# Kernel tuning notes

Measured on AMD Instinct MI355X. Metric: run time of the kernel, lower is better.

Reference implementation:

```python
import jax, jax.numpy as jnp
import numpy as np

B, N, E, D, H, C, FF, NQ, NCLS = 4, 1024, 512, 256, 2, 128, 1024, 4, 24
K_LOCAL, K_GLOBAL = 8, 7


def _ln(x, g, b, eps=1e-5):
    m = jnp.mean(x, -1, keepdims=True)
    v = jnp.mean((x - m) ** 2, -1, keepdims=True)
    return (x - m) * jax.lax.rsqrt(v + eps) * g + b


def _knn_mask(dist, k, exclude_self):
    # dist: [n, n]; returns bool mask[target, source] of k nearest sources per target
    n = dist.shape[-1]
    d = jnp.where(jnp.eye(n, dtype=bool), 1e9, dist) if exclude_self else dist
    idx = jax.lax.top_k(-d, k)[1]  # [n, k]
    rows = jnp.arange(n)[:, None]
    return jnp.zeros((n, n), dtype=bool).at[rows, idx].set(True)


def _mha(q, k, v, scale, extra_mask=None):
    # q: [B,Lq,H,C]  k,v: [B,Lk,H,C]
    logits = jnp.einsum('bqhc,bkhc->bhqk', q, k) * scale
    if extra_mask is not None:
        logits = logits + extra_mask
    a = jax.nn.softmax(logits, axis=-1)
    return jnp.einsum('bhqk,bkhc->bqhc', a, v)


def _forward(inputs, cellposes, sparse_rand, emb_W, emb_b, pe_tab, pe_W1, pe_b1, pe_W2, pe_b2,
             gat_W, gat_att_src, gat_att_dst, gat_b, ln_g, ln_b,
             tf_qkv_W, tf_qkv_b, tf_out_W, tf_out_b, tf_ff1_W, tf_ff1_b, tf_ff2_W, tf_ff2_b,
             tf_ln1_g, tf_ln1_b, tf_ln2_g, tf_ln2_b,
             query_embed, pool_in_W, pool_in_b, pool_out_W, pool_out_b,
             m1_W, m1_b, m_ln1_g, m_ln1_b, m2_W, m2_b, m_ln2_g, m_ln2_b, m3_W, m3_b,
             c1_W, c1_b, c2_W, c2_b, c3_W, c3_b, c4_W, c4_b, masks):
    # masks are all ones (full bags) -> key_padding_mask is all-False, no padding effect
    x = inputs @ emb_W.T + emb_b                                  # [B,N,D]
    # 2D position embedding: per-coordinate Embedding -> Linear -> ReLU -> Linear
    pos_idx = jnp.clip(cellposes, 0, 1000).astype(jnp.int32)      # [B,N,2]
    pes = []
    for c in range(2):
        e = pe_tab[c][pos_idx[..., c]]                            # [B,N,D//2]
        e = jax.nn.relu(e @ pe_W1[c].T + pe_b1[c]) @ pe_W2[c].T + pe_b2[c]
        pes.append(e)
    x = x + jnp.concatenate(pes, axis=-1)
    # kNN graph: local k=8 with self-loops + global k=7 without; coalesce('max') => edge-set union
    pm = cellposes.mean(axis=1, keepdims=True)
    ps = cellposes.std(axis=1, keepdims=True) + 1e-8
    pn = (cellposes - pm) / ps
    sq = jnp.sum((pn[:, :, None, :] - pn[:, None, :, :]) ** 2, axis=-1)
    dist = jax.lax.stop_gradient(jnp.sqrt(sq + 1e-12))            # [B,N,N]
    local = jax.vmap(lambda d: _knn_mask(d, K_LOCAL, False))(dist)
    glob = jax.vmap(lambda d: _knn_mask(d, K_GLOBAL, True))(dist)
    adj = local | glob                                            # [B, target, source]
    # GAT layers (PyG GATConv; edge weights are ignored since edge_dim=None)
    for l in range(gat_W.shape[0]):
        res = x
        h = (x @ gat_W[l].T).reshape(B, N, H, C)
        a_src = jnp.einsum('bnhc,hc->bnh', h, gat_att_src[l])
        a_dst = jnp.einsum('bnhc,hc->bnh', h, gat_att_dst[l])
        e = jax.nn.leaky_relu(a_dst[:, :, None, :] + a_src[:, None, :, :], 0.2)  # [B,t,s,H]
        e = jnp.where(adj[..., None], e, -1e9)
        a = jax.nn.softmax(e, axis=2)
        out = jnp.einsum('btsh,bshc->bthc', a, h).reshape(B, N, D) + gat_b[l]
        x = _ln(out + res, ln_g, ln_b)
    # TransformerEncoder: post-norm, ReLU FFN, batch_first, eval (no dropout)
    scale = 1.0 / jnp.sqrt(jnp.float32(C))
    for l in range(tf_qkv_W.shape[0]):
        qkv = x @ tf_qkv_W[l].T + tf_qkv_b[l]
        q, k, v = [t.reshape(B, N, H, C) for t in jnp.split(qkv, 3, axis=-1)]
        o = _mha(q, k, v, scale).reshape(B, N, D) @ tf_out_W[l].T + tf_out_b[l]
        x = _ln(x + o, tf_ln1_g[l], tf_ln1_b[l])
        ff = jax.nn.relu(x @ tf_ff1_W[l].T + tf_ff1_b[l]) @ tf_ff2_W[l].T + tf_ff2_b[l]
        x = _ln(x + ff, tf_ln2_g[l], tf_ln2_b[l])
    x = _ln(x, ln_g, ln_b)
    pooled_avg = x.mean(axis=1)                                   # AdaptiveAvgPool1d(1) == mean over seq
    # Sparse multihead attention pooling with learned queries
    queries = jnp.broadcast_to(query_embed[None], (B, NQ, D))
    attn_mask = jnp.where(sparse_rand < 0.3, 0.0, -1e9)           # [NQ, N]
    Wq, Wk, Wv = jnp.split(pool_in_W, 3, axis=0)
    bq, bk, bv = jnp.split(pool_in_b, 3, axis=0)
    q = (queries @ Wq.T + bq).reshape(B, NQ, H, C)
    k = (x @ Wk.T + bk).reshape(B, N, H, C)
    v = (x @ Wv.T + bv).reshape(B, N, H, C)
    pooled_att = _mha(q, k, v, scale, attn_mask[None, None]).reshape(B, NQ, D) @ pool_out_W.T + pool_out_b
    combined = jnp.concatenate([pooled_avg, pooled_att.reshape(B, NQ * D)], axis=-1)  # [B,(1+NQ)*D]
    h = jax.nn.relu(combined @ m1_W.T + m1_b)
    h = _ln(h, m_ln1_g, m_ln1_b)
    h = jax.nn.relu(h @ m2_W.T + m2_b)
    h = _ln(h, m_ln2_g, m_ln2_b)
    h = h @ m3_W.T + m3_b
    h = jax.nn.relu(h @ c1_W.T + c1_b)
    h = jax.nn.relu(h @ c2_W.T + c2_b)
    h = jax.nn.relu(h @ c3_W.T + c3_b)
    return h @ c4_W.T + c4_b                                      # [B, num_classes]


def setup_inputs() -> dict:
    key = jax.random.key(0)
    ks = iter(jax.random.split(key, 80))
    def W(shape, s=0.02):
        return jax.random.normal(next(ks), shape, jnp.float32) * s
    z = lambda *s: jnp.zeros(s, jnp.float32)
    o = lambda *s: jnp.ones(s, jnp.float32)
    return dict(
        inputs=jax.random.normal(next(ks), (B, N, E), jnp.float32),
        cellposes=jax.random.uniform(next(ks), (B, N, 2), jnp.float32) * 1000.0,
        sparse_rand=jax.random.uniform(next(ks), (NQ, N), jnp.float32),
        emb_W=W((D, E)), emb_b=z(D),
        pe_tab=W((2, 1001, D // 2)), pe_W1=W((2, D // 2, D // 2)), pe_b1=z(2, D // 2),
        pe_W2=W((2, D // 2, D // 2)), pe_b2=z(2, D // 2),
        gat_W=W((2, D, D)), gat_att_src=W((2, H, C)), gat_att_dst=W((2, H, C)), gat_b=z(2, D),
        ln_g=o(D), ln_b=z(D),
        tf_qkv_W=W((2, 3 * D, D)), tf_qkv_b=z(2, 3 * D), tf_out_W=W((2, D, D)), tf_out_b=z(2, D),
        tf_ff1_W=W((2, FF, D)), tf_ff1_b=z(2, FF), tf_ff2_W=W((2, D, FF)), tf_ff2_b=z(2, D),
        tf_ln1_g=o(2, D), tf_ln1_b=z(2, D), tf_ln2_g=o(2, D), tf_ln2_b=z(2, D),
        query_embed=W((NQ, D)),
        pool_in_W=W((3 * D, D)), pool_in_b=z(3 * D), pool_out_W=W((D, D)), pool_out_b=z(D),
        m1_W=W((1024, (1 + NQ) * D)), m1_b=z(1024), m_ln1_g=o(1024), m_ln1_b=z(1024),
        m2_W=W((1024, 1024)), m2_b=z(1024), m_ln2_g=o(1024), m_ln2_b=z(1024),
        m3_W=W((1024, 1024)), m3_b=z(1024),
        c1_W=W((1032, 1024)), c1_b=z(1032), c2_W=W((512, 1032)), c2_b=z(512),
        c3_W=W((256, 512)), c3_b=z(256), c4_W=W((NCLS, 256)), c4_b=z(NCLS),
        masks=jnp.ones((B, N), jnp.int32),
    )


def reference(inputs, cellposes, sparse_rand, emb_W, emb_b, pe_tab, pe_W1, pe_b1, pe_W2, pe_b2,
              gat_W, gat_att_src, gat_att_dst, gat_b, ln_g, ln_b,
              tf_qkv_W, tf_qkv_b, tf_out_W, tf_out_b, tf_ff1_W, tf_ff1_b, tf_ff2_W, tf_ff2_b,
              tf_ln1_g, tf_ln1_b, tf_ln2_g, tf_ln2_b,
              query_embed, pool_in_W, pool_in_b, pool_out_W, pool_out_b,
              m1_W, m1_b, m_ln1_g, m_ln1_b, m2_W, m2_b, m_ln2_g, m_ln2_b, m3_W, m3_b,
              c1_W, c1_b, c2_W, c2_b, c3_W, c3_b, c4_W, c4_b, masks):
    return _forward(inputs, cellposes, sparse_rand, emb_W, emb_b, pe_tab, pe_W1, pe_b1, pe_W2, pe_b2,
                    gat_W, gat_att_src, gat_att_dst, gat_b, ln_g, ln_b,
                    tf_qkv_W, tf_qkv_b, tf_out_W, tf_out_b, tf_ff1_W, tf_ff1_b, tf_ff2_W, tf_ff2_b,
                    tf_ln1_g, tf_ln1_b, tf_ln2_g, tf_ln2_b,
                    query_embed, pool_in_W, pool_in_b, pool_out_W, pool_out_b,
                    m1_W, m1_b, m_ln1_g, m_ln1_b, m2_W, m2_b, m_ln2_g, m_ln2_b, m3_W, m3_b,
                    c1_W, c1_b, c2_W, c2_b, c3_W, c3_b, c4_W, c4_b, masks)
```

## Files before the change

kernel.cpp:

```cpp
#include <hip/hip_runtime.h>
#include <hip/hip_bf16.h>


typedef __bf16 bf16x8 __attribute__((ext_vector_type(8)));
typedef float  f32x4  __attribute__((ext_vector_type(4)));

__device__ __forceinline__ ushort f2b(float f) {
  __hip_bfloat16 h = __float2bfloat16(f);
  return *(ushort*)&h;
}
__device__ __forceinline__ float b2f(ushort u) {
  union { unsigned i; float f; } v; v.i = ((unsigned)u) << 16; return v.f;
}

__device__ __forceinline__ float blk_sum256(float v, float* red) {
  int t = threadIdx.x;
  red[t] = v; __syncthreads();
  #pragma unroll
  for (int off = 128; off > 0; off >>= 1) {
    if (t < off) red[t] += red[t + off];
    __syncthreads();
  }
  float r = red[0]; __syncthreads();
  return r;
}

__global__ __launch_bounds__(256) void cvt_f2b(const float* __restrict__ src,
                                               ushort* __restrict__ dst, int n) {
  int i = (blockIdx.x * 256 + threadIdx.x) * 4;
  if (i >= n) return;
  float4 v = *(const float4*)(src + i);
  ushort4 o;
  o.x = f2b(v.x); o.y = f2b(v.y); o.z = f2b(v.z); o.w = f2b(v.w);
  *(ushort4*)(dst + i) = o;
}

__device__ __forceinline__ void stage8(const ushort* __restrict__ src, ushort* dst) {
  *(uint4*)dst = *(const uint4*)src;
}
__device__ __forceinline__ void stage8(const float* __restrict__ src, ushort* dst) {
  float4 a = ((const float4*)src)[0];
  float4 b = ((const float4*)src)[1];
  ushort4 o0, o1;
  o0.x = f2b(a.x); o0.y = f2b(a.y); o0.z = f2b(a.z); o0.w = f2b(a.w);
  o1.x = f2b(b.x); o1.y = f2b(b.y); o1.z = f2b(b.z); o1.w = f2b(b.w);
  *(ushort4*)dst = o0;
  *(ushort4*)(dst + 4) = o1;
}

template<typename CT, typename AT, typename WT, bool VSPLIT>
__global__ __launch_bounds__(256) void mfma_gemm(
    const AT* __restrict__ A, int lda,
    const WT* __restrict__ Bw, int ldb,
    const float* __restrict__ bias,
    CT* __restrict__ C, int ldc, int K, int relu,
    ushort* __restrict__ VT)
{
  __shared__ ushort As[64][40];
  __shared__ ushort Bs[128][40];
  int tid = threadIdx.x;
  int lane = tid & 63, wave = tid >> 6;
  int wm = wave >> 1, wn = wave & 1;
  int quad = lane >> 4, l16 = lane & 15;
  long mBase = blockIdx.y * 64, nBase = blockIdx.x * 128;

  f32x4 zero4 = {0.f, 0.f, 0.f, 0.f};
  f32x4 acc[2][4];
  #pragma unroll
  for (int i = 0; i < 2; i++)
    #pragma unroll
    for (int j = 0; j < 4; j++) acc[i][j] = zero4;

  for (int k0 = 0; k0 < K; k0 += 32) {
    {
      int r = tid >> 2, sg = (tid & 3) * 8;
      stage8(A + (mBase + r) * lda + k0 + sg, &As[r][sg]);
    }
    #pragma unroll
    for (int p = 0; p < 2; p++) {
      int idx = p * 256 + tid;
      int r = idx >> 2, sg = (idx & 3) * 8;
      stage8(Bw + (nBase + r) * ldb + k0 + sg, &Bs[r][sg]);
    }
    __syncthreads();
    bf16x8 af[2], bfr[4];
    #pragma unroll
    for (int i = 0; i < 2; i++)
      af[i] = *(const bf16x8*)&As[wm * 32 + i * 16 + l16][quad * 8];
    #pragma unroll
    for (int j = 0; j < 4; j++)
      bfr[j] = *(const bf16x8*)&Bs[wn * 64 + j * 16 + l16][quad * 8];
    #pragma unroll
    for (int i = 0; i < 2; i++)
      #pragma unroll
      for (int j = 0; j < 4; j++)
        acc[i][j] = __builtin_amdgcn_mfma_f32_16x16x32_bf16(af[i], bfr[j], acc[i][j], 0, 0, 0);
    __syncthreads();
  }
  #pragma unroll
  for (int i = 0; i < 2; i++) {
    #pragma unroll
    for (int j = 0; j < 4; j++) {
      long col = nBase + wn * 64 + j * 16 + l16;
      float bv = bias ? bias[col] : 0.f;
      long row0 = mBase + wm * 32 + i * 16 + quad * 4;
      if (VSPLIT && col >= 512) {
        int cm = (int)col - 512, hh = cm >> 7, cc = cm & 127;
        long bidx = row0 >> 10, n0 = row0 & 1023;
        ushort4 o;
        o.x = f2b(acc[i][j][0] + bv);
        o.y = f2b(acc[i][j][1] + bv);
        o.z = f2b(acc[i][j][2] + bv);
        o.w = f2b(acc[i][j][3] + bv);
        *(ushort4*)&VT[(((bidx * 2 + hh) * 128 + cc) << 10) + n0] = o;
      } else {
        #pragma unroll
        for (int r = 0; r < 4; r++) {
          float v = acc[i][j][r] + bv;
          if (relu) v = fmaxf(v, 0.f);
          if constexpr (sizeof(CT) == 2) C[(row0 + r) * ldc + col] = f2b(v);
          else                           C[(row0 + r) * ldc + col] = v;
        }
      }
    }
  }
}

template<typename CT, typename AT, typename WT>
static void mgemm(hipStream_t st, const AT* A, int lda, const WT* B, int ldb,
                  const float* bias, CT* C, int ldc, int M, int N, int K, int relu) {
  dim3 grid(N / 128, M / 64);
  mfma_gemm<CT, AT, WT, false><<<grid, 256, 0, st>>>(A, lda, B, ldb, bias, C, ldc, K, relu, nullptr);
}
template<typename AT, typename WT>
static void mgemm_vt(hipStream_t st, const AT* A, int lda, const WT* B, int ldb,
                     const float* bias, ushort* C, int ldc, int M, int N, int K, ushort* VT) {
  dim3 grid(N / 128, M / 64);
  mfma_gemm<ushort, AT, WT, true><<<grid, 256, 0, st>>>(A, lda, B, ldb, bias, C, ldc, K, 0, VT);
}

__global__ __launch_bounds__(256) void pos_mlp(
    const float* __restrict__ cellp, const float* __restrict__ tab,
    const float* __restrict__ W1, const float* __restrict__ b1,
    const float* __restrict__ W2, const float* __restrict__ b2,
    float* __restrict__ X)
{
  __shared__ ushort Es[64][136];
  __shared__ ushort Bs[128][136];
  __shared__ ushort H1s[64][136];
  int tid = threadIdx.x;
  int lane = tid & 63, wave = tid >> 6;
  int wm = wave >> 1, wn = wave & 1;
  int quad = lane >> 4, l16 = lane & 15;
  int r0 = blockIdx.x * 64, c = blockIdx.y;

  #pragma unroll
  for (int p = 0; p < 4; p++) {
    int idx = p * 256 + tid;
    int r = idx >> 4, c8 = (idx & 15) * 8;
    float pos = cellp[(r0 + r) * 2 + c];
    pos = fminf(fmaxf(pos, 0.f), 1000.f);
    int pi = (int)pos;
    stage8(tab + ((long)(c * 1001 + pi)) * 128 + c8, &Es[r][c8]);
  }
  #pragma unroll
  for (int p = 0; p < 8; p++) {
    int idx = p * 256 + tid;
    int r = idx >> 4, c8 = (idx & 15) * 8;
    stage8(W1 + ((long)(c * 128 + r)) * 128 + c8, &Bs[r][c8]);
  }
  __syncthreads();

  f32x4 zero4 = {0.f, 0.f, 0.f, 0.f};
  f32x4 acc[2][4];
  #pragma unroll
  for (int i = 0; i < 2; i++)
    #pragma unroll
    for (int j = 0; j < 4; j++) acc[i][j] = zero4;
  #pragma unroll
  for (int ks = 0; ks < 4; ks++) {
    bf16x8 af[2], bfr[4];
    #pragma unroll
    for (int i = 0; i < 2; i++)
      af[i] = *(const bf16x8*)&Es[wm * 32 + i * 16 + l16][ks * 32 + quad * 8];
    #pragma unroll
    for (int j = 0; j < 4; j++)
      bfr[j] = *(const bf16x8*)&Bs[wn * 64 + j * 16 + l16][ks * 32 + quad * 8];
    #pragma unroll
    for (int i = 0; i < 2; i++)
      #pragma unroll
      for (int j = 0; j < 4; j++)
        acc[i][j] = __builtin_amdgcn_mfma_f32_16x16x32_bf16(af[i], bfr[j], acc[i][j], 0, 0, 0);
  }
  #pragma unroll
  for (int i = 0; i < 2; i++)
    #pragma unroll
    for (int j = 0; j < 4; j++) {
      int col = wn * 64 + j * 16 + l16;
      float bv = b1[c * 128 + col];
      #pragma unroll
      for (int r = 0; r < 4; r++) {
        int row = wm * 32 + i * 16 + quad * 4 + r;
        H1s[row][col] = f2b(fmaxf(acc[i][j][r] + bv, 0.f));
      }
    }
  __syncthreads();
  #pragma unroll
  for (int p = 0; p < 8; p++) {
    int idx = p * 256 + tid;
    int r = idx >> 4, c8 = (idx & 15) * 8;
    stage8(W2 + ((long)(c * 128 + r)) * 128 + c8, &Bs[r][c8]);
  }
  __syncthreads();
  #pragma unroll
  for (int i = 0; i < 2; i++)
    #pragma unroll
    for (int j = 0; j < 4; j++) acc[i][j] = zero4;
  #pragma unroll
  for (int ks = 0; ks < 4; ks++) {
    bf16x8 af[2], bfr[4];
    #pragma unroll
    for (int i = 0; i < 2; i++)
      af[i] = *(const bf16x8*)&H1s[wm * 32 + i * 16 + l16][ks * 32 + quad * 8];
    #pragma unroll
    for (int j = 0; j < 4; j++)
      bfr[j] = *(const bf16x8*)&Bs[wn * 64 + j * 16 + l16][ks * 32 + quad * 8];
    #pragma unroll
    for (int i = 0; i < 2; i++)
      #pragma unroll
      for (int j = 0; j < 4; j++)
        acc[i][j] = __builtin_amdgcn_mfma_f32_16x16x32_bf16(af[i], bfr[j], acc[i][j], 0, 0, 0);
  }
  #pragma unroll
  for (int i = 0; i < 2; i++)
    #pragma unroll
    for (int j = 0; j < 4; j++) {
      int col = wn * 64 + j * 16 + l16;
      float bv = b2[c * 128 + col];
      #pragma unroll
      for (int r = 0; r < 4; r++) {
        long row = r0 + wm * 32 + i * 16 + quad * 4 + r;
        X[row * 256 + c * 128 + col] += acc[i][j][r] + bv;
      }
    }
}

template<int M_>
__global__ __launch_bounds__(256) void skinny_gemm(
    const float* __restrict__ A, int lda,
    const float* __restrict__ W, int K,
    float* __restrict__ P, int N, int slice)
{
  __shared__ float Asl[M_ * 192];
  __shared__ float Pr[4][M_][64];
  int tid = threadIdx.x;
  int ks = blockIdx.y;
  int kbeg = ks * slice;
  int kend = min(K, kbeg + slice);
  int sl = kend - kbeg;
  for (int idx = tid; idx < M_ * sl; idx += 256) {
    int m = idx / sl, k = idx - m * sl;
    Asl[m * sl + k] = A[(long)m * lda + kbeg + k];
  }
  __syncthreads();
  int n = blockIdx.x * 64 + (tid & 63);
  int sub = tid >> 6;
  int sl4 = (sl + 3) >> 2;
  int k0 = kbeg + sub * sl4;
  int k1 = min(kend, k0 + sl4);
  float acc[M_];
  #pragma unroll
  for (int m = 0; m < M_; m++) acc[m] = 0.f;
  if (n < N) {
    const float* wr = W + (long)n * K;
    for (int k = k0; k < k1; k++) {
      float w = wr[k];
      int kl = k - kbeg;
      #pragma unroll
      for (int m = 0; m < M_; m++) acc[m] += w * Asl[m * sl + kl];
    }
  }
  #pragma unroll
  for (int m = 0; m < M_; m++) Pr[sub][m][tid & 63] = acc[m];
  __syncthreads();
  if (sub == 0 && n < N) {
    #pragma unroll
    for (int m = 0; m < M_; m++) {
      float s = Pr[0][m][tid] + Pr[1][m][tid] + Pr[2][m][tid] + Pr[3][m][tid];
      P[((long)(ks * M_ + m)) * N + n] = s;
    }
  }
}

__global__ __launch_bounds__(256) void skinny_epi(
    const float* __restrict__ P, const float* __restrict__ bias,
    float* __restrict__ out, int M, int N, int KS, int relu)
{
  int idx = blockIdx.x * 256 + threadIdx.x;
  if (idx >= M * N) return;
  int m = idx / N, n = idx - m * N;
  float s = bias[n];
  for (int ks = 0; ks < KS; ks++) s += P[((long)(ks * M + m)) * N + n];
  if (relu) s = fmaxf(s, 0.f);
  out[(long)m * N + n] = s;
}

template<int M_>
static void sgemm(hipStream_t st, const float* A, int lda, const float* W, int K,
                  const float* bias, float* out, float* P, int N, int KS, int relu) {
  int slice = (K + KS - 1) / KS;
  dim3 grid((N + 63) / 64, KS);
  skinny_gemm<M_><<<grid, 256, 0, st>>>(A, lda, W, K, P, N, slice);
  skinny_epi<<<(M_ * N + 255) / 256, 256, 0, st>>>(P, bias, out, M_, N, KS, relu);
}

__global__ __launch_bounds__(256) void bag_stats(const float* __restrict__ cp, float* __restrict__ PN) {
  int b = blockIdx.x, tid = threadIdx.x;
  __shared__ float red[256];
  for (int c = 0; c < 2; c++) {
    float s = 0.f;
    for (int n = tid; n < 1024; n += 256) s += cp[((b << 10) + n) * 2 + c];
    float mean = blk_sum256(s, red) * (1.f / 1024.f);
    s = 0.f;
    for (int n = tid; n < 1024; n += 256) { float d = cp[((b << 10) + n) * 2 + c] - mean; s += d * d; }
    float var = blk_sum256(s, red) * (1.f / 1024.f);
    float inv = 1.f / (sqrtf(var) + 1e-8f);
    for (int n = tid; n < 1024; n += 256)
      PN[((b << 10) + n) * 2 + c] = (cp[((b << 10) + n) * 2 + c] - mean) * inv;
  }
}

__global__ __launch_bounds__(256) void knn_kernel(const float* __restrict__ PN, int* __restrict__ NBR) {
  int blk = blockIdx.x;
  int b = blk >> 5, tg = blk & 31;
  int tid = threadIdx.x;
  int tl = tid >> 3, chunk = tid & 7;
  __shared__ float px[1024], py[1024];
  __shared__ float candD[32][64];
  __shared__ int   candI[32][64];
  for (int i = tid; i < 1024; i += 256) {
    px[i] = PN[((b << 10) + i) * 2 + 0];
    py[i] = PN[((b << 10) + i) * 2 + 1];
  }
  __syncthreads();
  int t = tg * 32 + tl;
  float tx = px[t], ty = py[t];
  float d8[8]; int i8[8];
  #pragma unroll
  for (int i = 0; i < 8; i++) { d8[i] = 3.4e38f; i8[i] = 0x7fffffff; }
  int s0 = chunk * 128;
  for (int s = s0; s < s0 + 128; s++) {
    float dx = __fadd_rn(px[s], -tx), dy = __fadd_rn(py[s], -ty);
    float d2 = __fadd_rn(__fadd_rn(__fmul_rn(dx, dx), __fmul_rn(dy, dy)), 1e-12f);
    float d = sqrtf(d2);
    if (d < d8[7]) {
      d8[7] = d; i8[7] = s;
      #pragma unroll
      for (int p = 7; p > 0; p--) {
        if (d8[p] < d8[p - 1]) {
          float td = d8[p]; d8[p] = d8[p - 1]; d8[p - 1] = td;
          int ti = i8[p]; i8[p] = i8[p - 1]; i8[p - 1] = ti;
        }
      }
    }
  }
  #pragma unroll
  for (int i = 0; i < 8; i++) { candD[tl][chunk * 8 + i] = d8[i]; candI[tl][chunk * 8 + i] = i8[i]; }
  __syncthreads();
  if (chunk == 0) {
    float D[8]; int I[8];
    #pragma unroll
    for (int i = 0; i < 8; i++) { D[i] = candD[tl][i]; I[i] = candI[tl][i]; }
    for (int c = 1; c < 8; c++) {
      for (int j = 0; j < 8; j++) {
        float d = candD[tl][c * 8 + j]; int idx = candI[tl][c * 8 + j];
        bool better = (d < D[7]) || (d == D[7] && idx < I[7]);
        if (!better) break;
        D[7] = d; I[7] = idx;
        #pragma unroll
        for (int p = 7; p > 0; p--) {
          bool sw = (D[p] < D[p - 1]) || (D[p] == D[p - 1] && I[p] < I[p - 1]);
          if (sw) {
            float td = D[p]; D[p] = D[p - 1]; D[p - 1] = td;
            int ti = I[p]; I[p] = I[p - 1]; I[p - 1] = ti;
          }
        }
      }
    }
    #pragma unroll
    for (int i = 0; i < 8; i++) NBR[((long)((b << 10) + t)) * 8 + i] = I[i];
  }
}

__global__ __launch_bounds__(256) void gat_scores(const float* __restrict__ Hh,
    const float* __restrict__ asrcW, const float* __restrict__ adstW,
    float* __restrict__ ASRC, float* __restrict__ ADST)
{
  int row = blockIdx.x, tid = threadIdx.x;
  __shared__ float red[256];
  float v = Hh[(long)row * 256 + tid];
  float s1 = v * asrcW[tid];
  float s2 = v * adstW[tid];
  red[tid] = s1; __syncthreads();
  for (int off = 64; off > 0; off >>= 1) { if ((tid & 127) < off) red[tid] += red[tid + off]; __syncthreads(); }
  if ((tid & 127) == 0) ASRC[row * 2 + (tid >> 7)] = red[tid];
  __syncthreads();
  red[tid] = s2; __syncthreads();
  for (int off = 64; off > 0; off >>= 1) { if ((tid & 127) < off) red[tid] += red[tid + off]; __syncthreads(); }
  if ((tid & 127) == 0) ADST[row * 2 + (tid >> 7)] = red[tid];
}

__global__ __launch_bounds__(256) void gat_aggr_ln(
    const float* __restrict__ Hh, const float* __restrict__ ASRC, const float* __restrict__ ADST,
    const int* __restrict__ NBR, const float* __restrict__ gbias,
    const float* __restrict__ lng, const float* __restrict__ lnb,
    float* __restrict__ X, ushort* __restrict__ Xb)
{
  int row = blockIdx.x, tid = threadIdx.x;
  int b = row >> 10;
  __shared__ int nb[8];
  __shared__ float w[2][8];
  __shared__ float red[256];
  if (tid < 8) {
    int v = NBR[(long)row * 8 + tid];
    nb[tid] = min(max(v, 0), 1023);
  }
  __syncthreads();
  if (tid < 16) {
    int i = tid & 7, h = tid >> 3;
    float e = ADST[row * 2 + h] + ASRC[((b << 10) + nb[i]) * 2 + h];
    w[h][i] = (e >= 0.f) ? e : 0.2f * e;
  }
  __syncthreads();
  if (tid < 2) {
    float m = -3.4e38f;
    for (int i = 0; i < 8; i++) m = fmaxf(m, w[tid][i]);
    float s = 0.f;
    for (int i = 0; i < 8; i++) { float e = expf(w[tid][i] - m); w[tid][i] = e; s += e; }
    float inv = 1.f / s;
    for (int i = 0; i < 8; i++) w[tid][i] *= inv;
  }
  __syncthreads();
  int h = tid >> 7, c = tid & 127;
  float acc = 0.f;
  #pragma unroll
  for (int i = 0; i < 8; i++)
    acc += w[h][i] * Hh[((long)((b << 10) + nb[i])) * 256 + h * 128 + c];
  float v = acc + gbias[tid] + X[(long)row * 256 + tid];
  float mean = blk_sum256(v, red) * (1.f / 256.f);
  float dv = v - mean;
  float var = blk_sum256(dv * dv, red) * (1.f / 256.f);
  float o = dv * rsqrtf(var + 1e-5f) * lng[tid] + lnb[tid];
  X[(long)row * 256 + tid] = o;
  Xb[(long)row * 256 + tid] = f2b(o);
}

__global__ __launch_bounds__(256) void add_ln4(const float* __restrict__ res,
    const float* __restrict__ Yv, const float* __restrict__ g, const float* __restrict__ b,
    float* __restrict__ out, ushort* __restrict__ outb)
{
  int wave = threadIdx.x >> 6, lane = threadIdx.x & 63;
  long row = blockIdx.x * 4 + wave;
  const float* yr = Yv + row * 256;
  const float* rr = res ? res + row * 256 : nullptr;
  float v[4];
  float s = 0.f;
  #pragma unroll
  for (int i = 0; i < 4; i++) {
    int d = lane + i * 64;
    float x = yr[d];
    if (rr) x += rr[d];
    v[i] = x; s += x;
  }
  #pragma unroll
  for (int off = 32; off > 0; off >>= 1) s += __shfl_xor(s, off);
  float mean = s * (1.f / 256.f);
  float vs = 0.f;
  #pragma unroll
  for (int i = 0; i < 4; i++) { float dv = v[i] - mean; vs += dv * dv; }
  #pragma unroll
  for (int off = 32; off > 0; off >>= 1) vs += __shfl_xor(vs, off);
  float rstd = rsqrtf(vs * (1.f / 256.f) + 1e-5f);
  #pragma unroll
  for (int i = 0; i < 4; i++) {
    int d = lane + i * 64;
    float o = (v[i] - mean) * rstd * g[d] + b[d];
    out[row * 256 + d] = o;
    if (outb) outb[row * 256 + d] = f2b(o);
  }
}

__global__ __launch_bounds__(256) void add_ln_big(const float* __restrict__ Yv,
    const float* __restrict__ g, const float* __restrict__ b,
    float* __restrict__ out)
{
  int row = blockIdx.x, tid = threadIdx.x;
  __shared__ float red[256];
  float vals[4];
  float s = 0.f;
  #pragma unroll
  for (int i = 0; i < 4; i++) {
    int d = tid + (i << 8);
    float v = Yv[(long)row * 1024 + d];
    vals[i] = v; s += v;
  }
  float mean = blk_sum256(s, red) * (1.f / 1024.f);
  s = 0.f;
  #pragma unroll
  for (int i = 0; i < 4; i++) { float dv = vals[i] - mean; s += dv * dv; }
  float var = blk_sum256(s, red) * (1.f / 1024.f);
  float rstd = rsqrtf(var + 1e-5f);
  #pragma unroll
  for (int i = 0; i < 4; i++) {
    int d = tid + (i << 8);
    out[(long)row * 1024 + d] = (vals[i] - mean) * rstd * g[d] + b[d];
  }
}

__global__ __launch_bounds__(256) void flash_mfma(const ushort* __restrict__ QKV,
                                                  const ushort* __restrict__ VT,
                                                  ushort* __restrict__ O)
{
  const float scale = 0.08838834764831845f;
  int blk = blockIdx.x;
  int qt = blk & 15, bh = blk >> 4;
  int b = bh >> 1, h = bh & 1;
  const ushort* qkg = QKV + (long)b * 1024 * 768 + h * 128;
  const ushort* vtg = VT + ((long)bh << 17);

  __shared__ ushort Qs[64][136];
  __shared__ ushort Ks[64][136];
  __shared__ ushort Vt[128][72];
  __shared__ ushort Ps[4][16][72];

  int tid = threadIdx.x;
  int wave = tid >> 6, lane = tid & 63;
  int quad = lane >> 4, l16 = lane & 15;

  #pragma unroll
  for (int p = 0; p < 4; p++) {
    int idx = p * 256 + tid;
    int r = idx >> 4, c8 = (idx & 15) * 8;
    *(uint4*)&Qs[r][c8] = *(const uint4*)(qkg + (long)(qt * 64 + r) * 768 + c8);
  }
  __syncthreads();
  bf16x8 af[4];
  #pragma unroll
  for (int ks = 0; ks < 4; ks++)
    af[ks] = *(const bf16x8*)&Qs[wave * 16 + l16][ks * 32 + quad * 8];

  f32x4 Oacc[8];
  f32x4 zero4 = {0.f, 0.f, 0.f, 0.f};
  #pragma unroll
  for (int j = 0; j < 8; j++) Oacc[j] = zero4;
  float mr[4], lr[4];
  #pragma unroll
  for (int r = 0; r < 4; r++) { mr[r] = -3.4e38f; lr[r] = 0.f; }

  for (int kt = 0; kt < 16; kt++) {
    __syncthreads();
    #pragma unroll
    for (int p = 0; p < 4; p++) {
      int idx = p * 256 + tid;
      int r = idx >> 4, c8 = (idx & 15) * 8;
      *(uint4*)&Ks[r][c8] = *(const uint4*)(qkg + (long)(kt * 64 + r) * 768 + 256 + c8);
      int c = idx >> 3, k8 = (idx & 7) * 8;
      *(uint4*)&Vt[c][k8] = *(const uint4*)(vtg + ((long)c << 10) + kt * 64 + k8);
    }
    __syncthreads();
    f32x4 acc[4];
    #pragma unroll
    for (int j = 0; j < 4; j++) acc[j] = zero4;
    #pragma unroll
    for (int ks = 0; ks < 4; ks++) {
      #pragma unroll
      for (int j = 0; j < 4; j++) {
        bf16x8 kb = *(const bf16x8*)&Ks[j * 16 + l16][ks * 32 + quad * 8];
        acc[j] = __builtin_amdgcn_mfma_f32_16x16x32_bf16(af[ks], kb, acc[j], 0, 0, 0);
      }
    }
    float sv[4][4], tmax[4];
    #pragma unroll
    for (int r = 0; r < 4; r++) tmax[r] = -3.4e38f;
    #pragma unroll
    for (int j = 0; j < 4; j++)
      #pragma unroll
      for (int r = 0; r < 4; r++) {
        float x = acc[j][r] * scale;
        sv[j][r] = x;
        tmax[r] = fmaxf(tmax[r], x);
      }
    #pragma unroll
    for (int off = 1; off < 16; off <<= 1)
      #pragma unroll
      for (int r = 0; r < 4; r++) tmax[r] = fmaxf(tmax[r], __shfl_xor(tmax[r], off));
    float alpha[4], rsum[4];
    #pragma unroll
    for (int r = 0; r < 4; r++) {
      float mn = fmaxf(mr[r], tmax[r]);
      alpha[r] = expf(mr[r] - mn);
      mr[r] = mn;
      rsum[r] = 0.f;
    }
    #pragma unroll
    for (int j = 0; j < 4; j++)
      #pragma unroll
      for (int r = 0; r < 4; r++) {
        float p = expf(sv[j][r] - mr[r]);
        sv[j][r] = p;
        rsum[r] += p;
      }
    #pragma unroll
    for (int off = 1; off < 16; off <<= 1)
      #pragma unroll
      for (int r = 0; r < 4; r++) rsum[r] += __shfl_xor(rsum[r], off);
    #pragma unroll
    for (int r = 0; r < 4; r++) lr[r] = lr[r] * alpha[r] + rsum[r];
    #pragma unroll
    for (int j = 0; j < 4; j++)
      #pragma unroll
      for (int r = 0; r < 4; r++)
        Ps[wave][quad * 4 + r][j * 16 + l16] = f2b(sv[j][r]);
    #pragma unroll
    for (int jj = 0; jj < 8; jj++)
      #pragma unroll
      for (int r = 0; r < 4; r++) Oacc[jj][r] *= alpha[r];
    __syncthreads();
    #pragma unroll
    for (int s = 0; s < 2; s++) {
      bf16x8 pa = *(const bf16x8*)&Ps[wave][l16][s * 32 + quad * 8];
      #pragma unroll
      for (int jj = 0; jj < 8; jj++) {
        bf16x8 vb = *(const bf16x8*)&Vt[jj * 16 + l16][s * 32 + quad * 8];
        Oacc[jj] = __builtin_amdgcn_mfma_f32_16x16x32_bf16(pa, vb, Oacc[jj], 0, 0, 0);
      }
    }
  }
  long row0 = (long)b * 1024 + qt * 64 + wave * 16 + quad * 4;
  #pragma unroll
  for (int jj = 0; jj < 8; jj++) {
    int col = h * 128 + jj * 16 + l16;
    #pragma unroll
    for (int r = 0; r < 4; r++)
      O[(row0 + r) * 256 + col] = f2b(Oacc[jj][r] / lr[r]);
  }
}

__global__ __launch_bounds__(128) void pool_split(
    const float* __restrict__ qe, const float* __restrict__ pinW, const float* __restrict__ pinB,
    const float* __restrict__ srand, const ushort* __restrict__ KV,
    float* __restrict__ PM, float* __restrict__ PL, float* __restrict__ PO)
{
  int cid = blockIdx.x;
  int id = blockIdx.y;
  int h = id & 1, nq = (id >> 1) & 3, b = id >> 3;
  int tid = threadIdx.x;
  __shared__ float qs[128];
  __shared__ float eg[128];
  __shared__ float red[128];
  {
    float a = pinB[h * 128 + tid];
    const float* wr = pinW + ((long)(h * 128 + tid)) * 256;
    const float* qr = qe + nq * 256;
    for (int i = 0; i < 256; i++) a += qr[i] * wr[i];
    qs[tid] = a;
  }
  __syncthreads();
  const float scale = 0.08838834764831845f;
  int s = cid * 128 + tid;
  float d = 0.f;
  {
    const ushort* kr = KV + ((long)((b << 10) + s)) * 512 + h * 128;
    #pragma unroll
    for (int c8 = 0; c8 < 128; c8 += 8) {
      uint4 kv4 = *(const uint4*)(kr + c8);
      const ushort* kp = (const ushort*)&kv4;
      #pragma unroll
      for (int j = 0; j < 8; j++) d += qs[c8 + j] * b2f(kp[j]);
    }
  }
  float lg = d * scale + ((srand[nq * 1024 + s] < 0.3f) ? 0.f : -1e9f);
  red[tid] = lg; __syncthreads();
  for (int off = 64; off > 0; off >>= 1) { if (tid < off) red[tid] = fmaxf(red[tid], red[tid + off]); __syncthreads(); }
  float m = red[0]; __syncthreads();
  float e = expf(lg - m);
  eg[tid] = e;
  red[tid] = e; __syncthreads();
  for (int off = 64; off > 0; off >>= 1) { if (tid < off) red[tid] += red[tid + off]; __syncthreads(); }
  float l = red[0];
  __syncthreads();
  float o = 0.f;
  const ushort* vbase = KV + ((long)((b << 10) + cid * 128)) * 512 + 256 + h * 128 + tid;
  for (int ss = 0; ss < 128; ss++)
    o += eg[ss] * b2f(vbase[(long)ss * 512]);
  int part = id * 8 + cid;
  PO[(long)part * 128 + tid] = o;
  if (tid == 0) { PM[part] = m; PL[part] = l; }
}

__global__ __launch_bounds__(128) void pool_merge(
    const float* __restrict__ PM, const float* __restrict__ PL, const float* __restrict__ PO,
    float* __restrict__ ATTP)
{
  int id = blockIdx.x;
  int h = id & 1, nq = (id >> 1) & 3, b = id >> 3;
  int tid = threadIdx.x;
  float m = -3.4e38f;
  #pragma unroll
  for (int c = 0; c < 8; c++) m = fmaxf(m, PM[id * 8 + c]);
  float l = 0.f, o = 0.f;
  #pragma unroll
  for (int c = 0; c < 8; c++) {
    float w = expf(PM[id * 8 + c] - m);
    l += PL[id * 8 + c] * w;
    o += PO[(long)(id * 8 + c) * 128 + tid] * w;
  }
  ATTP[(b * 4 + nq) * 256 + h * 128 + tid] = o / l;
}

__global__ __launch_bounds__(256) void col_mean_part(const float* __restrict__ X,
                                                     float* __restrict__ PSUM)
{
  int blk = blockIdx.x;
  int b = blk >> 4, ch = blk & 15;
  int d = threadIdx.x;
  float s = 0.f;
  int n0 = ch * 64;
  const float* xr = X + ((long)((b << 10) + n0)) * 256 + d;
  #pragma unroll 4
  for (int n = 0; n < 64; n++) s += xr[(long)n * 256];
  PSUM[(long)blk * 256 + d] = s;
}

__global__ __launch_bounds__(256) void combined_merge(const float* __restrict__ PSUM,
    const float* __restrict__ ATTO, float* __restrict__ CMB)
{
  int b = blockIdx.x, d = threadIdx.x;
  float s = 0.f;
  #pragma unroll
  for (int ch = 0; ch < 16; ch++) s += PSUM[(long)(b * 16 + ch) * 256 + d];
  CMB[b * 1280 + d] = s * (1.f / 1024.f);
  #pragma unroll
  for (int q = 0; q < 4; q++)
    CMB[b * 1280 + 256 + q * 256 + d] = ATTO[(b * 4 + q) * 256 + d];
}

__global__ void store_out(const float* __restrict__ src, float* __restrict__ dst, int n) {
  int i = blockIdx.x * blockDim.x + threadIdx.x;
  if (i < n) dst[i] = src[i];
}
__global__ void fill_out_zero(float* __restrict__ dst, int n) {
  int i = blockIdx.x * blockDim.x + threadIdx.x;
  if (i < n) dst[i] = 0.f;
}

extern "C" void kernel_launch(void* const* d_in, const int* in_sizes, int n_in,
                              void* d_out, int out_size, void* d_ws, size_t ws_size,
                              hipStream_t stream)
{
  const float* inp      = (const float*)d_in[0];
  const float* cellp    = (const float*)d_in[1];
  const float* srand    = (const float*)d_in[2];
  const float* emb_W    = (const float*)d_in[3];
  const float* emb_b    = (const float*)d_in[4];
  const float* pe_tab   = (const float*)d_in[5];
  const float* pe_W1    = (const float*)d_in[6];
  const float* pe_b1    = (const float*)d_in[7];
  const float* pe_W2    = (const float*)d_in[8];
  const float* pe_b2    = (const float*)d_in[9];
  const float* gat_W    = (const float*)d_in[10];
  const float* gat_asrc = (const float*)d_in[11];
  const float* gat_adst = (const float*)d_in[12];
  const float* gat_b    = (const float*)d_in[13];
  const float* ln_g     = (const float*)d_in[14];
  const float* ln_b     = (const float*)d_in[15];
  const float* qkv_W    = (const float*)d_in[16];
  const float* qkv_b    = (const float*)d_in[17];
  const float* out_W    = (const float*)d_in[18];
  const float* out_b    = (const float*)d_in[19];
  const float* ff1_W    = (const float*)d_in[20];
  const float* ff1_b    = (const float*)d_in[21];
  const float* ff2_W    = (const float*)d_in[22];
  const float* ff2_b    = (const float*)d_in[23];
  const float* ln1_g    = (const float*)d_in[24];
  const float* ln1_b    = (const float*)d_in[25];
  const float* ln2_g    = (const float*)d_in[26];
  const float* ln2_b    = (const float*)d_in[27];
  const float* q_emb    = (const float*)d_in[28];
  const float* pin_W    = (const float*)d_in[29];
  const float* pin_b    = (const float*)d_in[30];
  const float* pout_W   = (const float*)d_in[31];
  const float* pout_b   = (const float*)d_in[32];
  const float* m1_W     = (const float*)d_in[33];
  const float* m1_b     = (const float*)d_in[34];
  const float* mln1_g   = (const float*)d_in[35];
  const float* mln1_b   = (const float*)d_in[36];
  const float* m2_W     = (const float*)d_in[37];
  const float* m2_b     = (const float*)d_in[38];
  const float* mln2_g   = (const float*)d_in[39];
  const float* mln2_b   = (const float*)d_in[40];
  const float* m3_W     = (const float*)d_in[41];
  const float* m3_b     = (const float*)d_in[42];
  const float* c1_W     = (const float*)d_in[43];
  const float* c1_b     = (const float*)d_in[44];
  const float* c2_W     = (const float*)d_in[45];
  const float* c2_b     = (const float*)d_in[46];
  const float* c3_W     = (const float*)d_in[47];
  const float* c3_b     = (const float*)d_in[48];
  const float* c4_W     = (const float*)d_in[49];
  const float* c4_b     = (const float*)d_in[50];
  (void)in_sizes; (void)n_in;

  char* base = (char*)d_ws;
  size_t off = 0;
  auto alloc = [&](size_t bytes) { void* p = base + off; off += (bytes + 255) & ~size_t(255); return p; };
  float* PN    = (float*)alloc(32768);
  float* AS    = (float*)alloc(32768);
  float* AD    = (float*)alloc(32768);
  float* ATTP  = (float*)alloc(16384);
  float* ATTO  = (float*)alloc(16384);
  float* CMB   = (float*)alloc(20480);
  float* Ha    = (float*)alloc(16384);
  float* Hb    = (float*)alloc(16384);
  float* Hc    = (float*)alloc(16640);
  float* Hd    = (float*)alloc(8192);
  float* He    = (float*)alloc(4096);
  float* Hf    = (float*)alloc(512);
  float* Pk    = (float*)alloc(262144);
  float* PPM   = (float*)alloc(1024);
  float* PPL   = (float*)alloc(1024);
  float* PPO   = (float*)alloc(131072);
  float* PSUM  = (float*)alloc(65536);
  int*   NBR   = (int*)alloc(131072);
  float* X     = (float*)alloc(4194304);
  ushort* Xb   = (ushort*)alloc(2097152);
  char*  Rq    = (char*)alloc(6291456);
  char*  Rf    = (char*)alloc(4194304);
  ushort* QKVb = (ushort*)Rq;
  float*  F2   = (float*)Rq;
  ushort* KVb  = (ushort*)Rq;
  ushort* Ob   = (ushort*)Rf;
  ushort* VT   = (ushort*)(Rf + 2097152);
  ushort* FFBb = (ushort*)Rf;
  float*  F1   = (float*)alloc(4194304);
  if (ws_size < off) { fill_out_zero<<<1, 128, 0, stream>>>((float*)d_out, out_size); return; }

  bag_stats<<<4, 256, 0, stream>>>(cellp, PN);
  knn_kernel<<<128, 256, 0, stream>>>(PN, NBR);

  mgemm<float>(stream, inp, 512, emb_W, 512, emb_b, X, 256, 4096, 256, 512, 0);
  pos_mlp<<<dim3(64, 2), 256, 0, stream>>>(cellp, pe_tab, pe_W1, pe_b1, pe_W2, pe_b2, X);
  cvt_f2b<<<1024, 256, 0, stream>>>(X, Xb, 4096 * 256);

  for (int l = 0; l < 2; l++) {
    mgemm<float>(stream, Xb, 256, gat_W + l * 65536, 256, (const float*)nullptr, F1, 256,
                 4096, 256, 256, 0);
    gat_scores<<<4096, 256, 0, stream>>>(F1, gat_asrc + l * 256, gat_adst + l * 256, AS, AD);
    gat_aggr_ln<<<4096, 256, 0, stream>>>(F1, AS, AD, NBR, gat_b + l * 256, ln_g, ln_b, X, Xb);
  }

  for (int l = 0; l < 2; l++) {
    mgemm_vt(stream, Xb, 256, qkv_W + (long)l * 768 * 256, 256, qkv_b + l * 768,
             QKVb, 768, 4096, 768, 256, VT);
    flash_mfma<<<256, 256, 0, stream>>>(QKVb, VT, Ob);
    mgemm<float>(stream, Ob, 256, out_W + l * 65536, 256, out_b + l * 256, F2, 256,
                 4096, 256, 256, 0);
    add_ln4<<<1024, 256, 0, stream>>>(X, F2, ln1_g + l * 256, ln1_b + l * 256, X, Xb);
    for (int ch = 0; ch < 2; ch++) {
      mgemm<ushort>(stream, Xb + (long)ch * 2048 * 256, 256, ff1_W + l * 262144, 256,
                    ff1_b + l * 1024, FFBb, 1024, 2048, 1024, 256, 1);
      mgemm<float>(stream, FFBb, 1024, ff2_W + l * 262144, 1024, ff2_b + l * 256,
                   F2 + (long)ch * 2048 * 256, 256, 2048, 256, 1024, 0);
    }
    add_ln4<<<1024, 256, 0, stream>>>(X, F2, ln2_g + l * 256, ln2_b + l * 256, X, Xb);
  }

  add_ln4<<<1024, 256, 0, stream>>>((const float*)nullptr, X, ln_g, ln_b, X, Xb);

  mgemm<ushort>(stream, Xb, 256, pin_W + 65536, 256, pin_b + 256, KVb, 512, 4096, 512, 256, 0);
  pool_split<<<dim3(8, 32), 128, 0, stream>>>(q_emb, pin_W, pin_b, srand, KVb, PPM, PPL, PPO);
  pool_merge<<<32, 128, 0, stream>>>(PPM, PPL, PPO, ATTP);
  sgemm<16>(stream, ATTP, 256, pout_W, 256, pout_b, ATTO, Pk, 256, 2, 0);
  col_mean_part<<<64, 256, 0, stream>>>(X, PSUM);
  combined_merge<<<4, 256, 0, stream>>>(PSUM, ATTO, CMB);

  sgemm<4>(stream, CMB, 1280, m1_W, 1280, m1_b, Ha, Pk, 1024, 8, 1);
  add_ln_big<<<4, 256, 0, stream>>>(Ha, mln1_g, mln1_b, Ha);
  sgemm<4>(stream, Ha, 1024, m2_W, 1024, m2_b, Hb, Pk, 1024, 8, 1);
  add_ln_big<<<4, 256, 0, stream>>>(Hb, mln2_g, mln2_b, Hb);
  sgemm<4>(stream, Hb, 1024, m3_W, 1024, m3_b, Ha, Pk, 1024, 8, 0);
  sgemm<4>(stream, Ha, 1024, c1_W, 1024, c1_b, Hc, Pk, 1032, 8, 1);
  sgemm<4>(stream, Hc, 1032, c2_W, 1032, c2_b, Hd, Pk, 512, 8, 1);
  sgemm<4>(stream, Hd, 512, c3_W, 512, c3_b, He, Pk, 256, 4, 1);
  sgemm<4>(stream, He, 256, c4_W, 256, c4_b, Hf, Pk, 24, 2, 0);
  store_out<<<1, 128, 0, stream>>>(Hf, (float*)d_out, out_size);
}
```

Baseline: 736.0 us.

## Split kNN search across 32 lanes per target with two-level merge

The kNN kernel now gives each target point 32 threads instead of 8, striding over sources, and launches 512 blocks instead of 128 so more CUs are occupied. The per-thread top-8 lists are merged in two stages (groups of 8 chunks, then 4 partial results) using a shared helper, and the candidate array is laid out so threads write to consecutive addresses. This cuts the serial scan length and the final merge depth per target. In exchange it adds an extra barrier and merge stage, and repeats the shared-memory load of all bag points in four times as many blocks.

```diff
diff --git a/kernel.cpp b/kernel.cpp
--- a/kernel.cpp
+++ b/kernel.cpp
@@ -330,26 +330,44 @@
   }
 }
 
+__device__ __forceinline__ void merge8(float* D, int* I,
+                                       const float* cd, const int* ci, int stride) {
+  #pragma unroll 1
+  for (int j = 0; j < 8; j++) {
+    float d = cd[j * stride]; int idx = ci[j * stride];
+    bool better = (d < D[7]) || (d == D[7] && idx < I[7]);
+    if (!better) break;
+    D[7] = d; I[7] = idx;
+    #pragma unroll
+    for (int p = 7; p > 0; p--) {
+      bool sw = (D[p] < D[p - 1]) || (D[p] == D[p - 1] && I[p] < I[p - 1]);
+      if (sw) {
+        float td = D[p]; D[p] = D[p - 1]; D[p - 1] = td;
+        int ti = I[p]; I[p] = I[p - 1]; I[p - 1] = ti;
+      }
+    }
+  }
+}
+
 __global__ __launch_bounds__(256) void knn_kernel(const float* __restrict__ PN, int* __restrict__ NBR) {
   int blk = blockIdx.x;
-  int b = blk >> 5, tg = blk & 31;
+  int b = blk >> 7, grp = blk & 127;
   int tid = threadIdx.x;
-  int tl = tid >> 3, chunk = tid & 7;
+  int tl = tid >> 5, chunk = tid & 31;
   __shared__ float px[1024], py[1024];
-  __shared__ float candD[32][64];
-  __shared__ int   candI[32][64];
+  __shared__ float candD[8][8][32];
+  __shared__ int   candI[8][8][32];
   for (int i = tid; i < 1024; i += 256) {
     px[i] = PN[((b << 10) + i) * 2 + 0];
     py[i] = PN[((b << 10) + i) * 2 + 1];
   }
   __syncthreads();
-  int t = tg * 32 + tl;
+  int t = grp * 8 + tl;
   float tx = px[t], ty = py[t];
   float d8[8]; int i8[8];
   #pragma unroll
   for (int i = 0; i < 8; i++) { d8[i] = 3.4e38f; i8[i] = 0x7fffffff; }
-  int s0 = chunk * 128;
-  for (int s = s0; s < s0 + 128; s++) {
+  for (int s = chunk; s < 1024; s += 32) {
     float dx = __fadd_rn(px[s], -tx), dy = __fadd_rn(py[s], -ty);
     float d2 = __fadd_rn(__fadd_rn(__fmul_rn(dx, dx), __fmul_rn(dy, dy)), 1e-12f);
     float d = sqrtf(d2);
@@ -365,28 +383,25 @@
     }
   }
   #pragma unroll
-  for (int i = 0; i < 8; i++) { candD[tl][chunk * 8 + i] = d8[i]; candI[tl][chunk * 8 + i] = i8[i]; }
+  for (int i = 0; i < 8; i++) { candD[tl][i][chunk] = d8[i]; candI[tl][i][chunk] = i8[i]; }
+  __syncthreads();
+  if ((chunk & 7) == 0) {
+    float D[8]; int I[8];
+    #pragma unroll
+    for (int i = 0; i < 8; i++) { D[i] = candD[tl][i][chunk]; I[i] = candI[tl][i][chunk]; }
+    for (int c = chunk + 1; c < chunk + 8; c++)
+      merge8(D, I, &candD[tl][0][c], &candI[tl][0][c], 32);
+    #pragma unroll
+    for (int i = 0; i < 8; i++) { candD[tl][i][chunk] = D[i]; candI[tl][i][chunk] = I[i]; }
+  }
   __syncthreads();
   if (chunk == 0) {
     float D[8]; int I[8];
     #pragma unroll
-    for (int i = 0; i < 8; i++) { D[i] = candD[tl][i]; I[i] = candI[tl][i]; }
-    for (int c = 1; c < 8; c++) {
-      for (int j = 0; j < 8; j++) {
-        float d = candD[tl][c * 8 + j]; int idx = candI[tl][c * 8 + j];
-        bool better = (d < D[7]) || (d == D[7] && idx < I[7]);
-        if (!better) break;
-        D[7] = d; I[7] = idx;
-        #pragma unroll
-        for (int p = 7; p > 0; p--) {
-          bool sw = (D[p] < D[p - 1]) || (D[p] == D[p - 1] && I[p] < I[p - 1]);
-          if (sw) {
-            float td = D[p]; D[p] = D[p - 1]; D[p - 1] = td;
-            int ti = I[p]; I[p] = I[p - 1]; I[p - 1] = ti;
-          }
-        }
-      }
-    }
+    for (int i = 0; i < 8; i++) { D[i] = candD[tl][i][0]; I[i] = candI[tl][i][0]; }
+    merge8(D, I, &candD[tl][0][8], &candI[tl][0][8], 32);
+    merge8(D, I, &candD[tl][0][16], &candI[tl][0][16], 32);
+    merge8(D, I, &candD[tl][0][24], &candI[tl][0][24], 32);
     #pragma unroll
     for (int i = 0; i < 8; i++) NBR[((long)((b << 10) + t)) * 8 + i] = I[i];
   }
@@ -846,7 +861,7 @@
   if (ws_size < off) { fill_out_zero<<<1, 128, 0, stream>>>((float*)d_out, out_size); return; }
 
   bag_stats<<<4, 256, 0, stream>>>(cellp, PN);
-  knn_kernel<<<128, 256, 0, stream>>>(PN, NBR);
+  knn_kernel<<<512, 256, 0, stream>>>(PN, NBR);
 
   mgemm<float>(stream, inp, 512, emb_W, 512, emb_b, X, 256, 4096, 256, 512, 0);
   pos_mlp<<<dim3(64, 2), 256, 0, stream>>>(cellp, pe_tab, pe_W1, pe_b1, pe_W2, pe_b2, X);
```

Measured after the change: 727.6 us. About the same (-1.1%).
